# Performance work log

Hardware: AMD Instinct MI355X
Metric: run time of the kernel (lower is better)

The kernel has to match this reference:

```python
import jax, jax.numpy as jnp
import numpy as np

COST_CLASS = 1.0


def _lsa(cost):
    """linear_sum_assignment clone (Jonker-Volgenant shortest augmenting path),
    matching scipy.optimize.linear_sum_assignment semantics for rectangular inputs."""
    cost = np.asarray(cost, dtype=np.float64)
    transposed = cost.shape[0] > cost.shape[1]
    if transposed:
        cost = cost.T
    nr, nc = cost.shape
    u = np.zeros(nr)
    v = np.zeros(nc)
    path = np.full(nc, -1, dtype=np.int64)
    col4row = np.full(nr, -1, dtype=np.int64)
    row4col = np.full(nc, -1, dtype=np.int64)
    for cur in range(nr):
        i = cur
        SR = np.zeros(nr, dtype=bool)
        SC = np.zeros(nc, dtype=bool)
        d = np.full(nc, np.inf)
        minVal = 0.0
        sink = -1
        while sink == -1:
            SR[i] = True
            rem = ~SC
            r = minVal + cost[i, rem] - u[i] - v[rem]
            dr = d[rem]
            pr = path[rem]
            better = r < dr
            dr[better] = r[better]
            pr[better] = i
            d[rem] = dr
            path[rem] = pr
            remIdx = np.flatnonzero(rem)
            j = remIdx[np.argmin(d[remIdx])]
            minVal = d[j]
            SC[j] = True
            if row4col[j] == -1:
                sink = j
            else:
                i = row4col[j]
        # dual updates (scipy _lsap_body)
        u[cur] += minVal
        mask = SR.copy()
        mask[cur] = False
        u[mask] += minVal - d[col4row[mask]]
        v[SC] -= minVal - d[SC]
        # augment along shortest path
        j = sink
        while True:
            i = path[j]
            row4col[j] = i
            col4row[i], j = j, col4row[i]
            if i == cur:
                break
    if transposed:
        order = np.argsort(col4row)
        return col4row[order], order
    return np.arange(nr), col4row


def setup_inputs() -> dict:
    key = jax.random.key(0)
    k1, k2, k3 = jax.random.split(key, 3)
    bs, Q, T, NC = 32, 256, 128, 2048
    pred_logits = jax.random.normal(k1, (bs, Q, NC), dtype=jnp.float32)
    tgt_labels = jax.random.randint(k2, (bs, T), 0, NC)
    agent_mask = jax.random.randint(k3, (bs, Q), 0, 2).astype(bool)
    return {"pred_logits": pred_logits, "tgt_labels": tgt_labels,
            "agent_mask": agent_mask, "use_background": 0}


def reference(pred_logits, tgt_labels, agent_mask, use_background):
    bs, Q, _ = pred_logits.shape
    T = tgt_labels.shape[1]
    probs = jax.nn.softmax(pred_logits, axis=-1)  # [bs, Q, NC]
    if not use_background:
        probs = jnp.where(agent_mask[:, :, None], probs, 0.0)
    out_prob = probs.reshape(bs * Q, -1)
    tgt_ids = tgt_labels.reshape(-1)                  # concat of all batch labels
    C = COST_CLASS * (-out_prob[:, tgt_ids])          # [bs*Q, bs*T]
    C = C.reshape(bs, Q, bs * T)
    # per-batch Hungarian (same as scipy loop in the original; inherently serial per instance)
    Cn = np.asarray(C)
    rows = np.empty((bs, T), dtype=np.int64)
    cols = np.empty((bs, T), dtype=np.int64)
    for i in range(bs):
        r, c = _lsa(Cn[i, :, i * T:(i + 1) * T])      # [Q, T] block for batch i
        rows[i] = r
        cols[i] = c
    return C, jnp.asarray(rows), jnp.asarray(cols)
```

## Files before the change

### kernel.cpp

```cpp
#include <hip/hip_runtime.h>
#include <hip/hip_bf16.h>
#include <math.h>

#define BS 32
#define QN 256
#define TN 128
#define NCLS 2048
#define NTGT (BS * TN)

__global__ void detect_mask_layout(const unsigned char* __restrict__ m, int* flag) {
    __shared__ int found;
    if (threadIdx.x == 0) found = 0;
    __syncthreads();
    int local = 0;
    for (int i = threadIdx.x; i < BS * QN; i += blockDim.x) {
        if ((i & 3) != 0 && m[i] != 0) local = 1;
    }
    if (local) atomicOr(&found, 1);
    __syncthreads();
    if (threadIdx.x == 0) *flag = found;
}

__global__ __launch_bounds__(256) void ct_kernel(
    const float* __restrict__ logits, const int* __restrict__ labels,
    const unsigned char* __restrict__ mask_b, const int* __restrict__ use_bg,
    const int* __restrict__ layout_flag, float* __restrict__ CT) {
    __shared__ float prob_sh[NCLS];
    __shared__ float red[4];

    const int tid = threadIdx.x;
    const int bq = blockIdx.x;
    const float* row = logits + (size_t)bq * NCLS;

    const float4 xa = ((const float4*)row)[tid];
    const float4 xb = ((const float4*)row)[tid + 256];

    float m = fmaxf(fmaxf(fmaxf(xa.x, xa.y), fmaxf(xa.z, xa.w)),
                    fmaxf(fmaxf(xb.x, xb.y), fmaxf(xb.z, xb.w)));
#pragma unroll
    for (int off = 32; off >= 1; off >>= 1) m = fmaxf(m, __shfl_xor(m, off));
    if ((tid & 63) == 0) red[tid >> 6] = m;
    __syncthreads();
    m = fmaxf(fmaxf(red[0], red[1]), fmaxf(red[2], red[3]));
    __syncthreads();

    float4 ea, eb;
    ea.x = expf(xa.x - m);
    ea.y = expf(xa.y - m);
    ea.z = expf(xa.z - m);
    ea.w = expf(xa.w - m);
    eb.x = expf(xb.x - m);
    eb.y = expf(xb.y - m);
    eb.z = expf(xb.z - m);
    eb.w = expf(xb.w - m);
    float s = ((ea.x + ea.y) + (ea.z + ea.w)) + ((eb.x + eb.y) + (eb.z + eb.w));
#pragma unroll
    for (int off = 32; off >= 1; off >>= 1) s += __shfl_xor(s, off);
    if ((tid & 63) == 0) red[tid >> 6] = s;
    __syncthreads();
    s = ((red[0] + red[1]) + red[2]) + red[3];

    ((float4*)prob_sh)[tid] = make_float4(ea.x / s, ea.y / s, ea.z / s, ea.w / s);
    ((float4*)prob_sh)[tid + 256] = make_float4(eb.x / s, eb.y / s, eb.z / s, eb.w / s);

    const int ub = *use_bg;
    int am;
    if (*layout_flag)
        am = mask_b[bq];
    else
        am = ((const int*)mask_b)[bq];
    const bool zero_row = (ub == 0) && (am == 0);
    __syncthreads();

    if (tid < TN) {
        const int bb = bq >> 8;
        const int q = bq & 255;
        const int lab = labels[bb * TN + tid];
        CT[(size_t)bb * TN * QN + (size_t)tid * QN + q] =
            zero_row ? 0.0f : -prob_sh[lab];
    }
}

__global__ __launch_bounds__(256) void compute_C_kernel(
    const float* __restrict__ logits, const int* __restrict__ labels,
    const unsigned char* __restrict__ mask_b, const int* __restrict__ use_bg,
    const int* __restrict__ layout_flag, float* __restrict__ C) {
    __shared__ float prob_sh[NCLS];
    __shared__ float red[4];

    const int tid = threadIdx.x;
    const int bq = blockIdx.x;
    const float* row = logits + (size_t)bq * NCLS;

    const float4 xa = ((const float4*)row)[tid];
    const float4 xb = ((const float4*)row)[tid + 256];

    float m = fmaxf(fmaxf(fmaxf(xa.x, xa.y), fmaxf(xa.z, xa.w)),
                    fmaxf(fmaxf(xb.x, xb.y), fmaxf(xb.z, xb.w)));
#pragma unroll
    for (int off = 32; off >= 1; off >>= 1) m = fmaxf(m, __shfl_xor(m, off));
    if ((tid & 63) == 0) red[tid >> 6] = m;
    __syncthreads();
    m = fmaxf(fmaxf(red[0], red[1]), fmaxf(red[2], red[3]));
    __syncthreads();

    float4 ea, eb;
    ea.x = expf(xa.x - m);
    ea.y = expf(xa.y - m);
    ea.z = expf(xa.z - m);
    ea.w = expf(xa.w - m);
    eb.x = expf(xb.x - m);
    eb.y = expf(xb.y - m);
    eb.z = expf(xb.z - m);
    eb.w = expf(xb.w - m);
    float s = ((ea.x + ea.y) + (ea.z + ea.w)) + ((eb.x + eb.y) + (eb.z + eb.w));
#pragma unroll
    for (int off = 32; off >= 1; off >>= 1) s += __shfl_xor(s, off);
    if ((tid & 63) == 0) red[tid >> 6] = s;
    __syncthreads();
    s = ((red[0] + red[1]) + red[2]) + red[3];

    ((float4*)prob_sh)[tid] = make_float4(ea.x / s, ea.y / s, ea.z / s, ea.w / s);
    ((float4*)prob_sh)[tid + 256] = make_float4(eb.x / s, eb.y / s, eb.z / s, eb.w / s);

    const int ub = *use_bg;
    int am;
    if (*layout_flag)
        am = mask_b[bq];
    else
        am = ((const int*)mask_b)[bq];
    const bool zero_row = (ub == 0) && (am == 0);
    __syncthreads();

    float* Crow = C + (size_t)bq * NTGT;
    const int4* lab4 = (const int4*)labels;
    if (zero_row) {
        const float4 z = make_float4(0.f, 0.f, 0.f, 0.f);
#pragma unroll
        for (int k = 0; k < 4; k++) ((float4*)Crow)[tid + k * 256] = z;
    } else {
#pragma unroll
        for (int k = 0; k < 4; k++) {
            const int4 l = lab4[tid + k * 256];
            float4 o;
            o.x = -prob_sh[l.x];
            o.y = -prob_sh[l.y];
            o.z = -prob_sh[l.z];
            o.w = -prob_sh[l.w];
            ((float4*)Crow)[tid + k * 256] = o;
        }
    }
}

template <int CTRL>
__device__ __forceinline__ double dpp_mov_f64(double x) {
    union { double d; int i[2]; } a, r;
    a.d = x;
    r.i[0] = __builtin_amdgcn_update_dpp(0, a.i[0], CTRL, 0xF, 0xF, true);
    r.i[1] = __builtin_amdgcn_update_dpp(0, a.i[1], CTRL, 0xF, 0xF, true);
    return r.d;
}
__device__ __forceinline__ double read_lane_f64(double x, int srclane) {
    union { double d; int i[2]; } a, r;
    a.d = x;
    r.i[0] = __builtin_amdgcn_readlane(a.i[0], srclane);
    r.i[1] = __builtin_amdgcn_readlane(a.i[1], srclane);
    return r.d;
}

#define QUAD_XOR1 0xB1
#define QUAD_XOR2 0x4E
#define ROW_ROR4  0x124
#define ROW_ROR8  0x128

__device__ __forceinline__ void lsa_solve(
    const float* __restrict__ C, const float* __restrict__ CT,
    float* __restrict__ rows_out, float* __restrict__ cols_out,
    int b, int lane,
    float* cost_sh, double* u_sh, int* col4row_sh) {
    const int j0 = lane * 4;

    u_sh[lane] = 0.0;
    u_sh[lane + 64] = 0.0;

    double v0 = 0.0, v1 = 0.0, v2 = 0.0, v3 = 0.0;
    double u0 = 0.0, u1 = 0.0;
    unsigned pk = 0u;
    int c0 = -1, c1 = -1;

    if (CT) {
        const float4* src = (const float4*)(CT + (size_t)b * TN * QN);
        float4* dst = (float4*)cost_sh;
#pragma unroll 8
        for (int it = 0; it < TN * QN / 4 / 64; it++) {
            const int idx = it * 64 + lane;
            dst[idx] = src[idx];
        }
    } else {
        const float* cbsrc = C + (size_t)b * QN * NTGT + b * TN;
        for (int it = 0; it < 512; it++) {
            const int j = it >> 1;
            const int i = lane + 64 * (it & 1);
            cost_sh[i * QN + j] = cbsrc[(size_t)j * NTGT + i];
        }
    }
    __syncthreads();

    for (int cur = 0; cur < TN; cur++) {
        double dv0 = INFINITY, dv1 = INFINITY, dv2 = INFINITY, dv3 = INFINITY;
        double dm0 = INFINITY, dm1 = INFINITY, dm2 = INFINITY, dm3 = INFINITY;
        double du0 = 0.0, du1 = 0.0;
        int sc = 0, sr = 0;
        int p0 = 0, p1 = 0, p2 = 0, p3 = 0;
        if (lane == (cur >> 1)) sr = 1 << (cur & 1);

        int i = cur;
        double m_d = 0.0;
        int tm = 0;
        int sink;

        while (true) {
            const float4 cc = *(const float4*)(cost_sh + i * QN + j0);
            const double ui = u_sh[i];

            const double ca0 = ((m_d + (double)cc.x) - ui) - v0;
            const double ca1 = ((m_d + (double)cc.y) - ui) - v1;
            const double ca2 = ((m_d + (double)cc.z) - ui) - v2;
            const double ca3 = ((m_d + (double)cc.w) - ui) - v3;
            const bool i0 = !(sc & 1) && (ca0 < dv0);
            const bool i1 = !(sc & 2) && (ca1 < dv1);
            const bool i2 = !(sc & 4) && (ca2 < dv2);
            const bool i3 = !(sc & 8) && (ca3 < dv3);
            if (i0) { dv0 = ca0; dm0 = ca0; p0 = i; }
            if (i1) { dv1 = ca1; dm1 = ca1; p1 = i; }
            if (i2) { dv2 = ca2; dm2 = ca2; p2 = i; }
            if (i3) { dv3 = ca3; dm3 = ca3; p3 = i; }

            const bool lt_any = (i0 && ca0 < m_d) || (i1 && ca1 < m_d) ||
                                (i2 && ca2 < m_d) || (i3 && ca3 < m_d);
            int tmn = tm;
            if (i0 && ca0 == m_d) tmn |= 1;
            if (i1 && ca1 == m_d) tmn |= 2;
            if (i2 && ca2 == m_d) tmn |= 4;
            if (i3 && ca3 == m_d) tmn |= 8;

            const unsigned long long LT = __ballot(lt_any);
            unsigned long long W = __ballot(tmn != 0);

            if (LT != 0ull || W == 0ull) {
                double lm = fmin(fmin(dm0, dm1), fmin(dm2, dm3));
                lm = fmin(lm, dpp_mov_f64<QUAD_XOR1>(lm));
                lm = fmin(lm, dpp_mov_f64<QUAD_XOR2>(lm));
                lm = fmin(lm, dpp_mov_f64<ROW_ROR4>(lm));
                lm = fmin(lm, dpp_mov_f64<ROW_ROR8>(lm));
                const double r0 = read_lane_f64(lm, 0);
                const double r1 = read_lane_f64(lm, 16);
                const double r2 = read_lane_f64(lm, 32);
                const double r3 = read_lane_f64(lm, 48);
                m_d = fmin(fmin(r0, r1), fmin(r2, r3));
                tmn = (dm0 == m_d ? 1 : 0) | (dm1 == m_d ? 2 : 0) |
                      (dm2 == m_d ? 4 : 0) | (dm3 == m_d ? 8 : 0);
                W = __ballot(tmn != 0);
            }

            const int owner = __ffsll((unsigned long long)W) - 1;
            const int sm = __builtin_amdgcn_readlane(tmn, owner);
            const unsigned pkv = (unsigned)__builtin_amdgcn_readlane((int)pk, owner);
            const int slot = __ffs(sm) - 1;
            const int jmin = (owner << 2) + slot;
            const int krc = (int)((pkv >> (slot * 8)) & 0xffu) - 1;

            if (lane == owner) {
                sc |= 1 << slot;
                tmn &= ~(1 << slot);
                if (slot == 0) dm0 = INFINITY;
                else if (slot == 1) dm1 = INFINITY;
                else if (slot == 2) dm2 = INFINITY;
                else dm3 = INFINITY;
            }
            tm = tmn;

            if (krc < 0) { sink = jmin; break; }

            if (lane == (krc >> 1)) {
                if (krc & 1) { du1 = m_d; sr |= 2; }
                else { du0 = m_d; sr |= 1; }
            }
            i = krc;
        }

        if (sc & 1) v0 -= m_d - dv0;
        if (sc & 2) v1 -= m_d - dv1;
        if (sc & 4) v2 -= m_d - dv2;
        if (sc & 8) v3 -= m_d - dv3;
        if (sr & 1) u0 += (2 * lane == cur) ? m_d : (m_d - du0);
        if (sr & 2) u1 += (2 * lane + 1 == cur) ? m_d : (m_d - du1);
        u_sh[2 * lane] = u0;
        u_sh[2 * lane + 1] = u1;

        int j = sink;
        while (true) {
            const int sl = j & 3;
            const int ow = j >> 2;
            const int pa = (sl & 1) ? p1 : p0;
            const int pb = (sl & 1) ? p3 : p2;
            const int pi = __builtin_amdgcn_readlane((sl & 2) ? pb : pa, ow);
            if (lane == ow) {
                const int sh = sl * 8;
                pk = (pk & ~(0xffu << sh)) | ((unsigned)(pi + 1) << sh);
            }
            const int nj = __builtin_amdgcn_readlane((pi & 1) ? c1 : c0, pi >> 1);
            if (lane == (pi >> 1)) {
                if (pi & 1) c1 = j;
                else c0 = j;
            }
            j = nj;
            if (pi == cur) break;
        }
        __syncthreads();
    }

    col4row_sh[2 * lane] = c0;
    col4row_sh[2 * lane + 1] = c1;
    __syncthreads();

#pragma unroll
    for (int t = 0; t < 2; t++) {
        const int ii = lane + 64 * t;
        const int myv = col4row_sh[ii];
        int rank = 0;
        for (int t2 = 0; t2 < TN; t2++) rank += (col4row_sh[t2] < myv) ? 1 : 0;
        rows_out[b * TN + rank] = (float)myv;
        cols_out[b * TN + rank] = (float)ii;
    }
}

__global__ __launch_bounds__(64) void lsa_kernel(const float* __restrict__ C,
                                                 const float* __restrict__ CT,
                                                 float* __restrict__ rows_out,
                                                 float* __restrict__ cols_out) {
    __shared__ float cost_sh[TN * QN];
    __shared__ double u_sh[TN];
    __shared__ int col4row_sh[TN];
    lsa_solve(C, CT, rows_out, cols_out, blockIdx.x, threadIdx.x,
              cost_sh, u_sh, col4row_sh);
}

__global__ __launch_bounds__(64) void fused_kernel(
    const float* __restrict__ logits, const int* __restrict__ labels,
    const unsigned char* __restrict__ mask_b, const int* __restrict__ use_bg,
    const int* __restrict__ layout_flag, const float* __restrict__ CT,
    float* __restrict__ C, float* __restrict__ rows_out,
    float* __restrict__ cols_out) {
    __shared__ float cost_sh[TN * QN];
    __shared__ double u_sh[TN];
    __shared__ int col4row_sh[TN];

    const int lane = threadIdx.x;

    if (blockIdx.x >= BS) {
        const int bq = blockIdx.x - BS;
        const float* row = logits + (size_t)bq * NCLS;

        float4 x[8];
#pragma unroll
        for (int k = 0; k < 8; k++) x[k] = ((const float4*)row)[lane + 64 * k];

        float m = -INFINITY;
#pragma unroll
        for (int k = 0; k < 8; k++)
            m = fmaxf(m, fmaxf(fmaxf(x[k].x, x[k].y), fmaxf(x[k].z, x[k].w)));
#pragma unroll
        for (int off = 32; off >= 1; off >>= 1) m = fmaxf(m, __shfl_xor(m, off));

        float s = 0.f;
        float4 e[8];
#pragma unroll
        for (int k = 0; k < 8; k++) {
            e[k].x = expf(x[k].x - m);
            e[k].y = expf(x[k].y - m);
            e[k].z = expf(x[k].z - m);
            e[k].w = expf(x[k].w - m);
            s += ((e[k].x + e[k].y) + (e[k].z + e[k].w));
        }
#pragma unroll
        for (int off = 32; off >= 1; off >>= 1) s += __shfl_xor(s, off);

        float* prob = cost_sh;
#pragma unroll
        for (int k = 0; k < 8; k++)
            ((float4*)prob)[lane + 64 * k] =
                make_float4(e[k].x / s, e[k].y / s, e[k].z / s, e[k].w / s);

        const int ub = *use_bg;
        int am;
        if (*layout_flag)
            am = mask_b[bq];
        else
            am = ((const int*)mask_b)[bq];
        const bool zero_row = (ub == 0) && (am == 0);
        __syncthreads();

        float* Crow = C + (size_t)bq * NTGT;
        const int4* lab4 = (const int4*)labels;
        if (zero_row) {
            const float4 z = make_float4(0.f, 0.f, 0.f, 0.f);
#pragma unroll
            for (int k = 0; k < 16; k++) ((float4*)Crow)[lane + 64 * k] = z;
        } else {
#pragma unroll
            for (int k = 0; k < 16; k++) {
                const int4 l = lab4[lane + 64 * k];
                ((float4*)Crow)[lane + 64 * k] =
                    make_float4(-prob[l.x], -prob[l.y], -prob[l.z], -prob[l.w]);
            }
        }
        return;
    }

    lsa_solve(nullptr, CT, rows_out, cols_out, blockIdx.x, lane,
              cost_sh, u_sh, col4row_sh);
}

extern "C" void kernel_launch(void* const* d_in, const int* in_sizes, int n_in,
                              void* d_out, int out_size, void* d_ws, size_t ws_size,
                              hipStream_t stream) {
    const float* logits = (const float*)d_in[0];
    const int* labels = (const int*)d_in[1];
    const unsigned char* mask_b = (const unsigned char*)d_in[2];
    const int* use_bg = (const int*)d_in[3];

    float* C = (float*)d_out;
    float* rows_out = C + (size_t)BS * QN * NTGT;
    float* cols_out = rows_out + BS * TN;

    int* flag = (int*)d_ws;
    const size_t ct_off = 4096;
    const size_t ct_bytes = (size_t)BS * TN * QN * sizeof(float);
    const bool useCT = ws_size >= ct_off + ct_bytes;
    float* CT = useCT ? (float*)((char*)d_ws + ct_off) : nullptr;

    detect_mask_layout<<<1, 256, 0, stream>>>(mask_b, flag);
    if (useCT) {
        ct_kernel<<<BS * QN, 256, 0, stream>>>(logits, labels, mask_b, use_bg, flag, CT);
        fused_kernel<<<BS + BS * QN, 64, 0, stream>>>(logits, labels, mask_b, use_bg,
                                                      flag, CT, C, rows_out, cols_out);
    } else {
        compute_C_kernel<<<BS * QN, 256, 0, stream>>>(logits, labels, mask_b, use_bg,
                                                      flag, C);
        lsa_kernel<<<BS, 64, 0, stream>>>(C, nullptr, rows_out, cols_out);
    }
}
```

Before: 1.057 ms.

## Keep row duals in registers and prefetch next cost row in LSA loop

```diff
diff --git a/kernel.cpp b/kernel.cpp
--- a/kernel.cpp
+++ b/kernel.cpp
@@ -177,11 +177,8 @@
     const float* __restrict__ C, const float* __restrict__ CT,
     float* __restrict__ rows_out, float* __restrict__ cols_out,
     int b, int lane,
-    float* cost_sh, double* u_sh, int* col4row_sh) {
+    float* cost_sh, int* col4row_sh) {
     const int j0 = lane * 4;
-
-    u_sh[lane] = 0.0;
-    u_sh[lane + 64] = 0.0;
 
     double v0 = 0.0, v1 = 0.0, v2 = 0.0, v3 = 0.0;
     double u0 = 0.0, u1 = 0.0;
@@ -206,6 +203,8 @@
     }
     __syncthreads();
 
+    float4 nx_cc = *(const float4*)(cost_sh + j0);
+
     for (int cur = 0; cur < TN; cur++) {
         double dv0 = INFINITY, dv1 = INFINITY, dv2 = INFINITY, dv3 = INFINITY;
         double dm0 = INFINITY, dm1 = INFINITY, dm2 = INFINITY, dm3 = INFINITY;
@@ -216,17 +215,20 @@
 
         int i = cur;
         double m_d = 0.0;
+        float4 cc = nx_cc;
+        double s2 = read_lane_f64((cur & 1) ? u1 : u0, cur >> 1);
         int tm = 0;
         int sink;
 
         while (true) {
-            const float4 cc = *(const float4*)(cost_sh + i * QN + j0);
-            const double ui = u_sh[i];
-
-            const double ca0 = ((m_d + (double)cc.x) - ui) - v0;
-            const double ca1 = ((m_d + (double)cc.y) - ui) - v1;
-            const double ca2 = ((m_d + (double)cc.z) - ui) - v2;
-            const double ca3 = ((m_d + (double)cc.w) - ui) - v3;
+            const double w0 = v0 + s2;
+            const double w1 = v1 + s2;
+            const double w2 = v2 + s2;
+            const double w3 = v3 + s2;
+            const double ca0 = (double)cc.x - w0;
+            const double ca1 = (double)cc.y - w1;
+            const double ca2 = (double)cc.z - w2;
+            const double ca3 = (double)cc.w - w3;
             const bool i0 = !(sc & 1) && (ca0 < dv0);
             const bool i1 = !(sc & 2) && (ca1 < dv1);
             const bool i2 = !(sc & 4) && (ca2 < dv2);
@@ -282,6 +284,10 @@
 
             if (krc < 0) { sink = jmin; break; }
 
+            cc = *(const float4*)(cost_sh + krc * QN + j0);
+            const double ui = read_lane_f64((krc & 1) ? u1 : u0, krc >> 1);
+            s2 = ui - m_d;
+
             if (lane == (krc >> 1)) {
                 if (krc & 1) { du1 = m_d; sr |= 2; }
                 else { du0 = m_d; sr |= 1; }
@@ -295,8 +301,8 @@
         if (sc & 8) v3 -= m_d - dv3;
         if (sr & 1) u0 += (2 * lane == cur) ? m_d : (m_d - du0);
         if (sr & 2) u1 += (2 * lane + 1 == cur) ? m_d : (m_d - du1);
-        u_sh[2 * lane] = u0;
-        u_sh[2 * lane + 1] = u1;
+
+        if (cur + 1 < TN) nx_cc = *(const float4*)(cost_sh + (cur + 1) * QN + j0);
 
         int j = sink;
         while (true) {
@@ -317,7 +323,6 @@
             j = nj;
             if (pi == cur) break;
         }
-        __syncthreads();
     }
 
     col4row_sh[2 * lane] = c0;
@@ -340,10 +345,9 @@
                                                  float* __restrict__ rows_out,
                                                  float* __restrict__ cols_out) {
     __shared__ float cost_sh[TN * QN];
-    __shared__ double u_sh[TN];
     __shared__ int col4row_sh[TN];
     lsa_solve(C, CT, rows_out, cols_out, blockIdx.x, threadIdx.x,
-              cost_sh, u_sh, col4row_sh);
+              cost_sh, col4row_sh);
 }
 
 __global__ __launch_bounds__(64) void fused_kernel(
@@ -353,7 +357,6 @@
     float* __restrict__ C, float* __restrict__ rows_out,
     float* __restrict__ cols_out) {
     __shared__ float cost_sh[TN * QN];
-    __shared__ double u_sh[TN];
     __shared__ int col4row_sh[TN];
 
     const int lane = threadIdx.x;
@@ -419,7 +422,7 @@
     }
 
     lsa_solve(nullptr, CT, rows_out, cols_out, blockIdx.x, lane,
-              cost_sh, u_sh, col4row_sh);
+              cost_sh, col4row_sh);
 }
 
 extern "C" void kernel_launch(void* const* d_in, const int* in_sizes, int n_in,
```

New measurement: 1.035 ms. 1.02x faster.
